# Performance work log

Hardware: AMD Instinct MI355X
Metric: run time of the kernel (lower is better)

The kernel has to match this reference:

```python
import jax, jax.numpy as jnp
import numpy as np

N = 100000
E = 1600000
C = 128
EPS = 1e-5


def setup_inputs() -> dict:
    key = jax.random.key(0)
    ks = jax.random.split(key, 12)
    x = jax.random.normal(ks[0], (N, C), dtype=jnp.float32)
    edges = jax.random.randint(ks[1], (2, E), 0, N, dtype=jnp.int64)
    s = 1.0 / np.sqrt(C)
    return {
        "x": x,
        "edges": edges,
        # GCNConv params
        "W1": jax.random.uniform(ks[2], (C, C), jnp.float32, -s, s),
        "b1": jnp.zeros((C,), jnp.float32),
        # GraphNorm params (shared between the two calls, as in the module)
        "gn_w": jnp.ones((C,), jnp.float32),
        "gn_b": jnp.zeros((C,), jnp.float32),
        "gn_ms": jnp.ones((C,), jnp.float32),  # mean_scale alpha
        # GATConv params (heads=1)
        "Wg": jax.random.uniform(ks[3], (C, C), jnp.float32, -s, s),
        "bg": jnp.zeros((C,), jnp.float32),
        "att_src": jax.random.uniform(ks[4], (C,), jnp.float32, -s, s),
        "att_dst": jax.random.uniform(ks[5], (C,), jnp.float32, -s, s),
    }


def _leaky(x, slope):
    return jnp.where(x >= 0, x, slope * x)


def _gcn_conv(x, src, dst, W, b):
    # PyG GCNConv with self-loops already appended to (src, dst)
    h = x @ W  # [N, C]
    deg = jnp.zeros((N,), x.dtype).at[dst].add(1.0)
    dinv = jax.lax.rsqrt(deg)  # deg >= 1 thanks to self-loops
    norm = dinv[src] * dinv[dst]  # [E+N]
    out = jax.ops.segment_sum(h[src] * norm[:, None], dst, num_segments=N)
    return out + b


def _graph_norm(x, w, b, ms):
    # PyG GraphNorm, single graph: center by alpha*mean, scale by std
    mean = jnp.mean(x, axis=0)
    out = x - ms * mean
    var = jnp.mean(out * out, axis=0)
    return w * out * jax.lax.rsqrt(var + EPS) + b


def _gat_conv(x, src, dst, W, b, att_src, att_dst):
    # PyG GATConv, heads=1, self-loops already appended
    h = x @ W  # [N, C]
    a_s = jnp.sum(h * att_src, axis=-1)  # [N]
    a_d = jnp.sum(h * att_dst, axis=-1)  # [N]
    e = _leaky(a_s[src] + a_d[dst], 0.2)  # [E+N]
    m = jax.ops.segment_max(e, dst, num_segments=N)
    e = jnp.exp(e - m[dst])
    denom = jax.ops.segment_sum(e, dst, num_segments=N)
    alpha = e / denom[dst]
    out = jax.ops.segment_sum(h[src] * alpha[:, None], dst, num_segments=N)
    return out + b


def reference(x, edges, W1, b1, gn_w, gn_b, gn_ms, Wg, bg, att_src, att_dst):
    loops = jnp.arange(N, dtype=edges.dtype)
    src = jnp.concatenate([edges[0], loops])
    dst = jnp.concatenate([edges[1], loops])

    t = _gcn_conv(x, src, dst, W1, b1)
    t = _graph_norm(t, gn_w, gn_b, gn_ms)
    t = _leaky(t, 0.01)  # nn.LeakyReLU default slope
    x = x + t

    t = _gat_conv(x, src, dst, Wg, bg, att_src, att_dst)
    t = _graph_norm(t, gn_w, gn_b, gn_ms)
    t = _leaky(t, 0.01)
    x = x + t
    return x
```

## Files before the change

### kernel.cpp

```cpp
#include <hip/hip_runtime.h>
#include <math.h>

#define NN 100000
#define NE 1600000
#define CH 128
#define TOTE (NE + NN)
#define EPSV 1e-5f
#define NB 98
#define NGB 1563

typedef __attribute__((ext_vector_type(8))) short short8;
typedef __attribute__((ext_vector_type(4))) float floatx4;

__device__ __forceinline__ float lrelu(float v, float s) { return v < 0.f ? v * s : v; }

__device__ __forceinline__ unsigned short f2bf(float f) {
    unsigned int u = __float_as_uint(f);
    u += 0x7FFF + ((u >> 16) & 1);
    return (unsigned short)(u >> 16);
}
__device__ __forceinline__ float bflo(unsigned int u) { return __uint_as_float(u << 16); }
__device__ __forceinline__ float bfhi(unsigned int u) { return __uint_as_float(u & 0xFFFF0000u); }

__global__ void k_init(int* __restrict__ deg, int* __restrict__ cursor, float* __restrict__ stats) {
    int i = blockIdx.x * 256 + threadIdx.x;
    if (i < NN) { deg[i] = 1; cursor[i] = 0; }
    if (i < 4096) stats[i] = 0.f;
}

__global__ void k_count(const int* __restrict__ edges, int* __restrict__ deg) {
    int i = blockIdx.x * 256 + threadIdx.x;
    if (i < NE) atomicAdd(&deg[edges[NE + i]], 1);
}

__global__ void k_scan1(const int* __restrict__ deg, int* __restrict__ bsum, float* __restrict__ dinv) {
    __shared__ int red[256];
    int t = threadIdx.x;
    int base = blockIdx.x * 1024 + t * 4;
    int s = 0;
#pragma unroll
    for (int j = 0; j < 4; j++) {
        int i = base + j;
        if (i < NN) { int d = deg[i]; s += d; dinv[i] = rsqrtf((float)d); }
    }
    red[t] = s; __syncthreads();
    for (int off = 128; off > 0; off >>= 1) { if (t < off) red[t] += red[t + off]; __syncthreads(); }
    if (t == 0) bsum[blockIdx.x] = red[0];
}

__global__ void k_scan2(const int* __restrict__ bsum, int* __restrict__ boff) {
    if (threadIdx.x == 0) {
        int acc = 0;
        for (int b = 0; b < NB; b++) { boff[b] = acc; acc += bsum[b]; }
    }
}

__global__ void k_scan3(const int* __restrict__ deg, const int* __restrict__ boff, int* __restrict__ rowptr) {
    __shared__ int sc[256];
    int t = threadIdx.x;
    int base = blockIdx.x * 1024 + t * 4;
    int d[4];
#pragma unroll
    for (int j = 0; j < 4; j++) { int i = base + j; d[j] = (i < NN) ? deg[i] : 0; }
    int local = d[0] + d[1] + d[2] + d[3];
    sc[t] = local; __syncthreads();
    for (int off = 1; off < 256; off <<= 1) {
        int v = (t >= off) ? sc[t - off] : 0;
        __syncthreads();
        sc[t] += v;
        __syncthreads();
    }
    int run = sc[t] - local + boff[blockIdx.x];
#pragma unroll
    for (int j = 0; j < 4; j++) {
        int i = base + j;
        if (i < NN) { rowptr[i] = run; run += d[j]; }
    }
    if (blockIdx.x == 0 && t == 0) rowptr[NN] = TOTE;
}

__global__ void k_fill(const int* __restrict__ edges, const int* __restrict__ rowptr,
                       int* __restrict__ cursor, int* __restrict__ csr) {
    int i = blockIdx.x * 256 + threadIdx.x;
    if (i < NE) {
        int s = edges[i], d = edges[NE + i];
        int pos = atomicAdd(&cursor[d], 1);
        csr[rowptr[d] + pos] = s;
    } else if (i < TOTE) {
        int v = i - NE;
        int pos = atomicAdd(&cursor[v], 1);
        csr[rowptr[v] + pos] = v;
    }
}

__global__ void k_wswz(const float* __restrict__ W1, const float* __restrict__ Wg,
                       unsigned short* __restrict__ Wsw1, unsigned short* __restrict__ Wsw2) {
    int t = blockIdx.x * 256 + threadIdx.x;
    if (t >= 16384) return;
    int j = t & 7, lane = (t >> 3) & 63, ks = (t >> 9) & 3, nt = t >> 11;
    int k = ks * 32 + (lane >> 4) * 8 + j;
    int n = nt * 16 + (lane & 15);
    Wsw1[t] = f2bf(W1[k * CH + n]);
    Wsw2[t] = f2bf(Wg[k * CH + n]);
}

__launch_bounds__(256, 4)
__global__ void k_gemm1(const float* __restrict__ X, const unsigned short* __restrict__ Wsw,
                        unsigned short* __restrict__ H) {
    __shared__ __align__(16) short Xl[64 * 136];
    int t = threadIdx.x, wave = t >> 6, lane = t & 63;
    int row0 = blockIdx.x * 64;
    {
        int r = t >> 2, q = t & 3;
        int gr = row0 + r;
        const float* Xr = X + (size_t)gr * CH;
#pragma unroll
        for (int j = 0; j < 4; j++) {
            int c0 = q * 32 + j * 8;
            float4 v0 = {0.f,0.f,0.f,0.f}, v1 = {0.f,0.f,0.f,0.f};
            if (gr < NN) { v0 = *(const float4*)&Xr[c0]; v1 = *(const float4*)&Xr[c0 + 4]; }
            short8 s;
            s[0]=f2bf(v0.x); s[1]=f2bf(v0.y); s[2]=f2bf(v0.z); s[3]=f2bf(v0.w);
            s[4]=f2bf(v1.x); s[5]=f2bf(v1.y); s[6]=f2bf(v1.z); s[7]=f2bf(v1.w);
            *(short8*)&Xl[r * 136 + c0] = s;
        }
    }
    __syncthreads();
    floatx4 acc[8];
#pragma unroll
    for (int nt = 0; nt < 8; nt++) acc[nt] = (floatx4){0.f, 0.f, 0.f, 0.f};
    int arow = wave * 16 + (lane & 15);
    int koff = (lane >> 4) * 8;
#pragma unroll
    for (int ks = 0; ks < 4; ks++) {
        short8 af = *(short8*)&Xl[arow * 136 + ks * 32 + koff];
#pragma unroll
        for (int nt = 0; nt < 8; nt++) {
            short8 bf = *(const short8*)&Wsw[((nt * 4 + ks) * 64 + lane) * 8];
            acc[nt] = __builtin_amdgcn_mfma_f32_16x16x32_bf16(af, bf, acc[nt], 0, 0, 0);
        }
    }
    int orow0 = row0 + wave * 16 + (lane >> 4) * 4;
    int ocol = lane & 15;
#pragma unroll
    for (int nt = 0; nt < 8; nt++) {
#pragma unroll
        for (int r = 0; r < 4; r++) {
            int row = orow0 + r;
            if (row < NN) H[(size_t)row * CH + nt * 16 + ocol] = f2bf(acc[nt][r]);
        }
    }
}

__launch_bounds__(256)
__global__ void k_gcn_agg(const unsigned short* __restrict__ H, const int* __restrict__ csr,
                          const int* __restrict__ rowptr, const float* __restrict__ dinv,
                          const float* __restrict__ b1, unsigned short* __restrict__ T,
                          float* __restrict__ stats) {
    __shared__ float red_s[4][128], red_q[4][128];
    int t = threadIdx.x, wave = t >> 6, lane = t & 63;
    int g = lane >> 4, sl = lane & 15;
    float4 bb0 = *(const float4*)&b1[sl * 8];
    float4 bb1 = *(const float4*)&b1[sl * 8 + 4];
    float bias[8] = {bb0.x, bb0.y, bb0.z, bb0.w, bb1.x, bb1.y, bb1.z, bb1.w};
    float ssum[8], ssq[8];
#pragma unroll
    for (int j = 0; j < 8; j++) { ssum[j] = 0.f; ssq[j] = 0.f; }
    for (int node = blockIdx.x * 4 + wave; node < NN; node += gridDim.x * 4) {
        int beg = rowptr[node], end = rowptr[node + 1];
        float di = dinv[node];
        float acc[8];
#pragma unroll
        for (int j = 0; j < 8; j++) acc[j] = 0.f;
        int kk0 = beg + g;
        int s_cur = csr[kk0 < end ? kk0 : end - 1];
        for (int k = beg; k < end; k += 4) {
            int kn = k + 4 + g;
            int s_next = csr[kn < end ? kn : end - 1];
            bool valid = (k + g) < end;
            float w = valid ? dinv[s_cur] : 0.f;
            uint4 u = *(const uint4*)&H[(size_t)s_cur * CH + sl * 8];
            acc[0] = fmaf(w, bflo(u.x), acc[0]); acc[1] = fmaf(w, bfhi(u.x), acc[1]);
            acc[2] = fmaf(w, bflo(u.y), acc[2]); acc[3] = fmaf(w, bfhi(u.y), acc[3]);
            acc[4] = fmaf(w, bflo(u.z), acc[4]); acc[5] = fmaf(w, bfhi(u.z), acc[5]);
            acc[6] = fmaf(w, bflo(u.w), acc[6]); acc[7] = fmaf(w, bfhi(u.w), acc[7]);
            s_cur = s_next;
        }
#pragma unroll
        for (int j = 0; j < 8; j++) {
            acc[j] += __shfl_xor(acc[j], 16);
            acc[j] += __shfl_xor(acc[j], 32);
        }
        if (lane < 16) {
            short8 sv;
#pragma unroll
            for (int j = 0; j < 8; j++) {
                float tv = fmaf(di, acc[j], bias[j]);
                sv[j] = (short)f2bf(tv);
                ssum[j] += tv; ssq[j] = fmaf(tv, tv, ssq[j]);
            }
            *(short8*)&T[(size_t)node * CH + sl * 8] = sv;
        }
    }
    if (lane < 16) {
#pragma unroll
        for (int j = 0; j < 8; j++) { red_s[wave][sl * 8 + j] = ssum[j]; red_q[wave][sl * 8 + j] = ssq[j]; }
    }
    __syncthreads();
    if (t < 128) {
        float s = 0.f, q = 0.f;
        for (int w2 = 0; w2 < 4; w2++) { s += red_s[w2][t]; q += red_q[w2][t]; }
        float* bank = stats + (blockIdx.x & 7) * 256;
        atomicAdd(&bank[t], s);
        atomicAdd(&bank[128 + t], q);
    }
}

__global__ void k_fin(const float* __restrict__ stats, const float* __restrict__ gw,
                      const float* __restrict__ gb, const float* __restrict__ gms,
                      float* __restrict__ alpha, float* __restrict__ beta) {
    int c = threadIdx.x;
    float s = 0.f, q = 0.f;
    for (int b = 0; b < 8; b++) { s += stats[b * 256 + c]; q += stats[b * 256 + 128 + c]; }
    float mean = s * (1.f / NN);
    float ctr = gms[c] * mean;
    float var = q * (1.f / NN) - 2.f * ctr * mean + ctr * ctr;
    float al = gw[c] * rsqrtf(var + EPSV);
    alpha[c] = al;
    beta[c] = gb[c] - al * ctr;
}

__launch_bounds__(256, 4)
__global__ void k_gemm2(const float* __restrict__ X, const unsigned short* __restrict__ T,
                        const unsigned short* __restrict__ Wsw, const float* __restrict__ alpha,
                        const float* __restrict__ beta, const float* __restrict__ attS,
                        const float* __restrict__ attD, float* __restrict__ X1out,
                        unsigned short* __restrict__ H, float* __restrict__ a_s, float* __restrict__ a_d) {
    __shared__ __align__(16) short Xl[64 * 136];
    int t = threadIdx.x, wave = t >> 6, lane = t & 63;
    int row0 = blockIdx.x * 64;
    {
        int r = t >> 2, q = t & 3;
        int gr = row0 + r;
        size_t base = (size_t)gr * CH;
#pragma unroll
        for (int j = 0; j < 4; j++) {
            int c0 = q * 32 + j * 8;
            float4 v0 = {0.f,0.f,0.f,0.f}, v1 = {0.f,0.f,0.f,0.f};
            if (gr < NN) {
                float4 xv0 = *(const float4*)&X[base + c0];
                float4 xv1 = *(const float4*)&X[base + c0 + 4];
                uint4 tu = *(const uint4*)&T[base + c0];
                float4 al0 = *(const float4*)&alpha[c0];
                float4 al1 = *(const float4*)&alpha[c0 + 4];
                float4 be0 = *(const float4*)&beta[c0];
                float4 be1 = *(const float4*)&beta[c0 + 4];
                v0.x = xv0.x + lrelu(fmaf(al0.x, bflo(tu.x), be0.x), 0.01f);
                v0.y = xv0.y + lrelu(fmaf(al0.y, bfhi(tu.x), be0.y), 0.01f);
                v0.z = xv0.z + lrelu(fmaf(al0.z, bflo(tu.y), be0.z), 0.01f);
                v0.w = xv0.w + lrelu(fmaf(al0.w, bfhi(tu.y), be0.w), 0.01f);
                v1.x = xv1.x + lrelu(fmaf(al1.x, bflo(tu.z), be1.x), 0.01f);
                v1.y = xv1.y + lrelu(fmaf(al1.y, bfhi(tu.z), be1.y), 0.01f);
                v1.z = xv1.z + lrelu(fmaf(al1.z, bflo(tu.w), be1.z), 0.01f);
                v1.w = xv1.w + lrelu(fmaf(al1.w, bfhi(tu.w), be1.w), 0.01f);
                *(float4*)&X1out[base + c0] = v0;
                *(float4*)&X1out[base + c0 + 4] = v1;
            }
            short8 s;
            s[0]=f2bf(v0.x); s[1]=f2bf(v0.y); s[2]=f2bf(v0.z); s[3]=f2bf(v0.w);
            s[4]=f2bf(v1.x); s[5]=f2bf(v1.y); s[6]=f2bf(v1.z); s[7]=f2bf(v1.w);
            *(short8*)&Xl[r * 136 + c0] = s;
        }
    }
    __syncthreads();
    floatx4 acc[8];
#pragma unroll
    for (int nt = 0; nt < 8; nt++) acc[nt] = (floatx4){0.f, 0.f, 0.f, 0.f};
    int arow = wave * 16 + (lane & 15);
    int koff = (lane >> 4) * 8;
#pragma unroll
    for (int ks = 0; ks < 4; ks++) {
        short8 af = *(short8*)&Xl[arow * 136 + ks * 32 + koff];
#pragma unroll
        for (int nt = 0; nt < 8; nt++) {
            short8 bf = *(const short8*)&Wsw[((nt * 4 + ks) * 64 + lane) * 8];
            acc[nt] = __builtin_amdgcn_mfma_f32_16x16x32_bf16(af, bf, acc[nt], 0, 0, 0);
        }
    }
    int orow0 = row0 + wave * 16 + (lane >> 4) * 4;
    int ocol = lane & 15;
    float ps[4] = {0.f, 0.f, 0.f, 0.f}, pd[4] = {0.f, 0.f, 0.f, 0.f};
#pragma unroll
    for (int nt = 0; nt < 8; nt++) {
        float as_v = attS[nt * 16 + ocol];
        float ad_v = attD[nt * 16 + ocol];
#pragma unroll
        for (int r = 0; r < 4; r++) {
            int row = orow0 + r;
            if (row < NN) H[(size_t)row * CH + nt * 16 + ocol] = f2bf(acc[nt][r]);
            ps[r] = fmaf(acc[nt][r], as_v, ps[r]);
            pd[r] = fmaf(acc[nt][r], ad_v, pd[r]);
        }
    }
#pragma unroll
    for (int off = 1; off < 16; off <<= 1) {
#pragma unroll
        for (int r = 0; r < 4; r++) {
            ps[r] += __shfl_xor(ps[r], off);
            pd[r] += __shfl_xor(pd[r], off);
        }
    }
    if ((lane & 15) == 0) {
#pragma unroll
        for (int r = 0; r < 4; r++) {
            int row = orow0 + r;
            if (row < NN) { a_s[row] = ps[r]; a_d[row] = pd[r]; }
        }
    }
}

__launch_bounds__(256)
__global__ void k_gat_agg(const unsigned short* __restrict__ H, const int* __restrict__ csr,
                          const int* __restrict__ rowptr, const float* __restrict__ a_s,
                          const float* __restrict__ a_d, const float* __restrict__ bg,
                          unsigned short* __restrict__ T, float* __restrict__ stats) {
    __shared__ float red_s[4][128], red_q[4][128];
    int t = threadIdx.x, wave = t >> 6, lane = t & 63;
    int g = lane >> 4, sl = lane & 15;
    float4 bb0 = *(const float4*)&bg[sl * 8];
    float4 bb1 = *(const float4*)&bg[sl * 8 + 4];
    float bias[8] = {bb0.x, bb0.y, bb0.z, bb0.w, bb1.x, bb1.y, bb1.z, bb1.w};
    float ssum[8], ssq[8];
#pragma unroll
    for (int j = 0; j < 8; j++) { ssum[j] = 0.f; ssq[j] = 0.f; }
    for (int node = blockIdx.x * 4 + wave; node < NN; node += gridDim.x * 4) {
        int beg = rowptr[node], end = rowptr[node + 1];
        float adI = a_d[node];
        float acc[8];
#pragma unroll
        for (int j = 0; j < 8; j++) acc[j] = 0.f;
        float den = 0.f;
        int kk0 = beg + g;
        int s_cur = csr[kk0 < end ? kk0 : end - 1];
        for (int k = beg; k < end; k += 4) {
            int kn = k + 4 + g;
            int s_next = csr[kn < end ? kn : end - 1];
            bool valid = (k + g) < end;
            float e = lrelu(a_s[s_cur] + adI, 0.2f);
            float wgt = valid ? __expf(e) : 0.f;
            den += wgt;
            uint4 u = *(const uint4*)&H[(size_t)s_cur * CH + sl * 8];
            acc[0] = fmaf(wgt, bflo(u.x), acc[0]); acc[1] = fmaf(wgt, bfhi(u.x), acc[1]);
            acc[2] = fmaf(wgt, bflo(u.y), acc[2]); acc[3] = fmaf(wgt, bfhi(u.y), acc[3]);
            acc[4] = fmaf(wgt, bflo(u.z), acc[4]); acc[5] = fmaf(wgt, bfhi(u.z), acc[5]);
            acc[6] = fmaf(wgt, bflo(u.w), acc[6]); acc[7] = fmaf(wgt, bfhi(u.w), acc[7]);
            s_cur = s_next;
        }
#pragma unroll
        for (int j = 0; j < 8; j++) {
            acc[j] += __shfl_xor(acc[j], 16);
            acc[j] += __shfl_xor(acc[j], 32);
        }
        den += __shfl_xor(den, 16);
        den += __shfl_xor(den, 32);
        float inv = 1.f / den;
        if (lane < 16) {
            short8 sv;
#pragma unroll
            for (int j = 0; j < 8; j++) {
                float tv = fmaf(acc[j], inv, bias[j]);
                sv[j] = (short)f2bf(tv);
                ssum[j] += tv; ssq[j] = fmaf(tv, tv, ssq[j]);
            }
            *(short8*)&T[(size_t)node * CH + sl * 8] = sv;
        }
    }
    if (lane < 16) {
#pragma unroll
        for (int j = 0; j < 8; j++) { red_s[wave][sl * 8 + j] = ssum[j]; red_q[wave][sl * 8 + j] = ssq[j]; }
    }
    __syncthreads();
    if (t < 128) {
        float s = 0.f, q = 0.f;
        for (int w2 = 0; w2 < 4; w2++) { s += red_s[w2][t]; q += red_q[w2][t]; }
        float* bank = stats + (blockIdx.x & 7) * 256;
        atomicAdd(&bank[t], s);
        atomicAdd(&bank[128 + t], q);
    }
}

__global__ void k_final(const unsigned short* __restrict__ T, const float* __restrict__ alpha,
                        const float* __restrict__ beta, float* __restrict__ out) {
    size_t i = (size_t)(blockIdx.x * 256 + threadIdx.x) * 4;
    if (i >= (size_t)NN * CH) return;
    int c = (int)(i & (CH - 1));
    uint2 tu = *(const uint2*)&T[i];
    float4 av = *(const float4*)&alpha[c];
    float4 bv = *(const float4*)&beta[c];
    float4 o = *(float4*)&out[i];
    o.x += lrelu(fmaf(av.x, bflo(tu.x), bv.x), 0.01f);
    o.y += lrelu(fmaf(av.y, bfhi(tu.x), bv.y), 0.01f);
    o.z += lrelu(fmaf(av.z, bflo(tu.y), bv.z), 0.01f);
    o.w += lrelu(fmaf(av.w, bfhi(tu.y), bv.w), 0.01f);
    *(float4*)&out[i] = o;
}

extern "C" void kernel_launch(void* const* d_in, const int* in_sizes, int n_in,
                              void* d_out, int out_size, void* d_ws, size_t ws_size,
                              hipStream_t stream) {
    const float* x    = (const float*)d_in[0];
    const int*   edges= (const int*)d_in[1];
    const float* W1   = (const float*)d_in[2];
    const float* b1   = (const float*)d_in[3];
    const float* gw   = (const float*)d_in[4];
    const float* gb   = (const float*)d_in[5];
    const float* gms  = (const float*)d_in[6];
    const float* Wg   = (const float*)d_in[7];
    const float* bg   = (const float*)d_in[8];
    const float* attS = (const float*)d_in[9];
    const float* attD = (const float*)d_in[10];
    float* out = (float*)d_out;

    char* w = (char*)d_ws;
    size_t o = 0;
    unsigned short* H = (unsigned short*)(w + o); o += (size_t)NN * CH * 2;
    unsigned short* T = (unsigned short*)(w + o); o += (size_t)NN * CH * 2;
    int*   csr    = (int*)(w + o);   o += (size_t)TOTE * 4;
    int*   rowptr = (int*)(w + o);   o += (size_t)(NN + 64) * 4;
    int*   deg    = (int*)(w + o);   o += (size_t)NN * 4;
    int*   cursor = (int*)(w + o);   o += (size_t)NN * 4;
    float* dinv   = (float*)(w + o); o += (size_t)NN * 4;
    float* a_s    = (float*)(w + o); o += (size_t)NN * 4;
    float* a_d    = (float*)(w + o); o += (size_t)NN * 4;
    int*   bsum   = (int*)(w + o);   o += 512;
    int*   boff   = (int*)(w + o);   o += 512;
    float* stats  = (float*)(w + o); o += 4096 * 4;
    float* alpha1 = (float*)(w + o); o += 512;
    float* beta1  = (float*)(w + o); o += 512;
    float* alpha2 = (float*)(w + o); o += 512;
    float* beta2  = (float*)(w + o); o += 512;
    unsigned short* Wsw1 = (unsigned short*)(w + o); o += 16384 * 2;
    unsigned short* Wsw2 = (unsigned short*)(w + o); o += 16384 * 2;

    k_init <<<(NN + 255) / 256, 256, 0, stream>>>(deg, cursor, stats);
    k_count<<<(NE + 255) / 256, 256, 0, stream>>>(edges, deg);
    k_scan1<<<NB, 256, 0, stream>>>(deg, bsum, dinv);
    k_scan2<<<1, 32, 0, stream>>>(bsum, boff);
    k_scan3<<<NB, 256, 0, stream>>>(deg, boff, rowptr);
    k_fill <<<(TOTE + 255) / 256, 256, 0, stream>>>(edges, rowptr, cursor, csr);
    k_wswz <<<64, 256, 0, stream>>>(W1, Wg, Wsw1, Wsw2);

    k_gemm1  <<<NGB, 256, 0, stream>>>(x, Wsw1, H);
    k_gcn_agg<<<2048, 256, 0, stream>>>(H, csr, rowptr, dinv, b1, T, stats);
    k_fin    <<<1, 128, 0, stream>>>(stats, gw, gb, gms, alpha1, beta1);

    k_gemm2  <<<NGB, 256, 0, stream>>>(x, T, Wsw2, alpha1, beta1, attS, attD, out, H, a_s, a_d);
    k_gat_agg<<<2048, 256, 0, stream>>>(H, csr, rowptr, a_s, a_d, bg, T, stats + 2048);
    k_fin    <<<1, 128, 0, stream>>>(stats + 2048, gw, gb, gms, alpha2, beta2);

    k_final<<<(NN * CH / 4 + 255) / 256, 256, 0, stream>>>(T, alpha2, beta2, out);
}
```

Before: 525.2 us.

## Widen aggregation gathers, vectorize CSR build, cache bf16 x for second GEMM

```diff
diff --git a/kernel.cpp b/kernel.cpp
--- a/kernel.cpp
+++ b/kernel.cpp
@@ -11,6 +11,7 @@
 
 typedef __attribute__((ext_vector_type(8))) short short8;
 typedef __attribute__((ext_vector_type(4))) float floatx4;
+typedef __attribute__((ext_vector_type(4))) int intx4;
 
 __device__ __forceinline__ float lrelu(float v, float s) { return v < 0.f ? v * s : v; }
 
@@ -30,7 +31,12 @@
 
 __global__ void k_count(const int* __restrict__ edges, int* __restrict__ deg) {
     int i = blockIdx.x * 256 + threadIdx.x;
-    if (i < NE) atomicAdd(&deg[edges[NE + i]], 1);
+    int base = i * 4;
+    if (base < NE) {
+        intx4 d = __builtin_nontemporal_load((const intx4*)&edges[NE + base]);
+        atomicAdd(&deg[d.x], 1); atomicAdd(&deg[d.y], 1);
+        atomicAdd(&deg[d.z], 1); atomicAdd(&deg[d.w], 1);
+    }
 }
 
 __global__ void k_scan1(const int* __restrict__ deg, int* __restrict__ bsum, float* __restrict__ dinv) {
@@ -49,10 +55,17 @@
 }
 
 __global__ void k_scan2(const int* __restrict__ bsum, int* __restrict__ boff) {
-    if (threadIdx.x == 0) {
-        int acc = 0;
-        for (int b = 0; b < NB; b++) { boff[b] = acc; acc += bsum[b]; }
-    }
+    __shared__ int sc[128];
+    int t = threadIdx.x;
+    int v = (t < NB) ? bsum[t] : 0;
+    sc[t] = v; __syncthreads();
+    for (int off = 1; off < 128; off <<= 1) {
+        int u = (t >= off) ? sc[t - off] : 0;
+        __syncthreads();
+        sc[t] += u;
+        __syncthreads();
+    }
+    if (t < NB) boff[t] = sc[t] - v;
 }
 
 __global__ void k_scan3(const int* __restrict__ deg, const int* __restrict__ boff, int* __restrict__ rowptr) {
@@ -80,16 +93,27 @@
 }
 
 __global__ void k_fill(const int* __restrict__ edges, const int* __restrict__ rowptr,
-                       int* __restrict__ cursor, int* __restrict__ csr) {
+                       int* __restrict__ cursor, int* __restrict__ csr, int lo, int hi) {
     int i = blockIdx.x * 256 + threadIdx.x;
-    if (i < NE) {
-        int s = edges[i], d = edges[NE + i];
-        int pos = atomicAdd(&cursor[d], 1);
-        csr[rowptr[d] + pos] = s;
-    } else if (i < TOTE) {
-        int v = i - NE;
-        int pos = atomicAdd(&cursor[v], 1);
-        csr[rowptr[v] + pos] = v;
+    int base = i * 4;
+    if (base < NE) {
+        intx4 d = __builtin_nontemporal_load((const intx4*)&edges[NE + base]);
+        intx4 s = __builtin_nontemporal_load((const intx4*)&edges[base]);
+#pragma unroll
+        for (int j = 0; j < 4; j++) {
+            int dj = (j == 0) ? d.x : (j == 1) ? d.y : (j == 2) ? d.z : d.w;
+            int sj = (j == 0) ? s.x : (j == 1) ? s.y : (j == 2) ? s.z : s.w;
+            if (dj >= lo && dj < hi) {
+                int pos = atomicAdd(&cursor[dj], 1);
+                csr[rowptr[dj] + pos] = sj;
+            }
+        }
+    } else {
+        int v = i - NE / 4;
+        if (v < NN && v >= lo && v < hi) {
+            int pos = atomicAdd(&cursor[v], 1);
+            csr[rowptr[v] + pos] = v;
+        }
     }
 }
 
@@ -106,7 +130,7 @@
 
 __launch_bounds__(256, 4)
 __global__ void k_gemm1(const float* __restrict__ X, const unsigned short* __restrict__ Wsw,
-                        unsigned short* __restrict__ H) {
+                        unsigned short* __restrict__ H, unsigned short* __restrict__ Xb) {
     __shared__ __align__(16) short Xl[64 * 136];
     int t = threadIdx.x, wave = t >> 6, lane = t & 63;
     int row0 = blockIdx.x * 64;
@@ -123,6 +147,7 @@
             s[0]=f2bf(v0.x); s[1]=f2bf(v0.y); s[2]=f2bf(v0.z); s[3]=f2bf(v0.w);
             s[4]=f2bf(v1.x); s[5]=f2bf(v1.y); s[6]=f2bf(v1.z); s[7]=f2bf(v1.w);
             *(short8*)&Xl[r * 136 + c0] = s;
+            if (gr < NN) *(short8*)&Xb[(size_t)gr * CH + c0] = s;
         }
     }
     __syncthreads();
@@ -159,52 +184,74 @@
                           float* __restrict__ stats) {
     __shared__ float red_s[4][128], red_q[4][128];
     int t = threadIdx.x, wave = t >> 6, lane = t & 63;
-    int g = lane >> 4, sl = lane & 15;
-    float4 bb0 = *(const float4*)&b1[sl * 8];
-    float4 bb1 = *(const float4*)&b1[sl * 8 + 4];
-    float bias[8] = {bb0.x, bb0.y, bb0.z, bb0.w, bb1.x, bb1.y, bb1.z, bb1.w};
-    float ssum[8], ssq[8];
-#pragma unroll
-    for (int j = 0; j < 8; j++) { ssum[j] = 0.f; ssq[j] = 0.f; }
+    int g = lane >> 3, sl = lane & 7;
+    float bias[16];
+    {
+        float4 b0 = *(const float4*)&b1[sl * 16];
+        float4 b1v = *(const float4*)&b1[sl * 16 + 4];
+        float4 b2 = *(const float4*)&b1[sl * 16 + 8];
+        float4 b3 = *(const float4*)&b1[sl * 16 + 12];
+        bias[0]=b0.x; bias[1]=b0.y; bias[2]=b0.z; bias[3]=b0.w;
+        bias[4]=b1v.x; bias[5]=b1v.y; bias[6]=b1v.z; bias[7]=b1v.w;
+        bias[8]=b2.x; bias[9]=b2.y; bias[10]=b2.z; bias[11]=b2.w;
+        bias[12]=b3.x; bias[13]=b3.y; bias[14]=b3.z; bias[15]=b3.w;
+    }
+    float ssum[16], ssq[16];
+#pragma unroll
+    for (int j = 0; j < 16; j++) { ssum[j] = 0.f; ssq[j] = 0.f; }
     for (int node = blockIdx.x * 4 + wave; node < NN; node += gridDim.x * 4) {
         int beg = rowptr[node], end = rowptr[node + 1];
         float di = dinv[node];
-        float acc[8];
-#pragma unroll
-        for (int j = 0; j < 8; j++) acc[j] = 0.f;
+        float acc[16];
+#pragma unroll
+        for (int j = 0; j < 16; j++) acc[j] = 0.f;
         int kk0 = beg + g;
         int s_cur = csr[kk0 < end ? kk0 : end - 1];
-        for (int k = beg; k < end; k += 4) {
-            int kn = k + 4 + g;
+        for (int k = beg; k < end; k += 8) {
+            int kn = k + 8 + g;
             int s_next = csr[kn < end ? kn : end - 1];
             bool valid = (k + g) < end;
             float w = valid ? dinv[s_cur] : 0.f;
-            uint4 u = *(const uint4*)&H[(size_t)s_cur * CH + sl * 8];
-            acc[0] = fmaf(w, bflo(u.x), acc[0]); acc[1] = fmaf(w, bfhi(u.x), acc[1]);
-            acc[2] = fmaf(w, bflo(u.y), acc[2]); acc[3] = fmaf(w, bfhi(u.y), acc[3]);
-            acc[4] = fmaf(w, bflo(u.z), acc[4]); acc[5] = fmaf(w, bfhi(u.z), acc[5]);
-            acc[6] = fmaf(w, bflo(u.w), acc[6]); acc[7] = fmaf(w, bfhi(u.w), acc[7]);
+            const unsigned short* Hp = &H[(size_t)s_cur * CH + sl * 16];
+            uint4 u0 = *(const uint4*)Hp;
+            uint4 u1 = *(const uint4*)(Hp + 8);
+            acc[0] = fmaf(w, bflo(u0.x), acc[0]);  acc[1] = fmaf(w, bfhi(u0.x), acc[1]);
+            acc[2] = fmaf(w, bflo(u0.y), acc[2]);  acc[3] = fmaf(w, bfhi(u0.y), acc[3]);
+            acc[4] = fmaf(w, bflo(u0.z), acc[4]);  acc[5] = fmaf(w, bfhi(u0.z), acc[5]);
+            acc[6] = fmaf(w, bflo(u0.w), acc[6]);  acc[7] = fmaf(w, bfhi(u0.w), acc[7]);
+            acc[8] = fmaf(w, bflo(u1.x), acc[8]);  acc[9] = fmaf(w, bfhi(u1.x), acc[9]);
+            acc[10] = fmaf(w, bflo(u1.y), acc[10]); acc[11] = fmaf(w, bfhi(u1.y), acc[11]);
+            acc[12] = fmaf(w, bflo(u1.z), acc[12]); acc[13] = fmaf(w, bfhi(u1.z), acc[13]);
+            acc[14] = fmaf(w, bflo(u1.w), acc[14]); acc[15] = fmaf(w, bfhi(u1.w), acc[15]);
             s_cur = s_next;
         }
 #pragma unroll
-        for (int j = 0; j < 8; j++) {
+        for (int j = 0; j < 16; j++) {
+            acc[j] += __shfl_xor(acc[j], 8);
             acc[j] += __shfl_xor(acc[j], 16);
             acc[j] += __shfl_xor(acc[j], 32);
         }
-        if (lane < 16) {
-            short8 sv;
+        if (g == 0) {
+            short8 sv0, sv1;
 #pragma unroll
             for (int j = 0; j < 8; j++) {
                 float tv = fmaf(di, acc[j], bias[j]);
-                sv[j] = (short)f2bf(tv);
+                sv0[j] = (short)f2bf(tv);
                 ssum[j] += tv; ssq[j] = fmaf(tv, tv, ssq[j]);
             }
-            *(short8*)&T[(size_t)node * CH + sl * 8] = sv;
-        }
-    }
-    if (lane < 16) {
-#pragma unroll
-        for (int j = 0; j < 8; j++) { red_s[wave][sl * 8 + j] = ssum[j]; red_q[wave][sl * 8 + j] = ssq[j]; }
+#pragma unroll
+            for (int j = 0; j < 8; j++) {
+                float tv = fmaf(di, acc[8 + j], bias[8 + j]);
+                sv1[j] = (short)f2bf(tv);
+                ssum[8 + j] += tv; ssq[8 + j] = fmaf(tv, tv, ssq[8 + j]);
+            }
+            *(short8*)&T[(size_t)node * CH + sl * 16] = sv0;
+            *(short8*)&T[(size_t)node * CH + sl * 16 + 8] = sv1;
+        }
+    }
+    if (g == 0) {
+#pragma unroll
+        for (int j = 0; j < 16; j++) { red_s[wave][sl * 16 + j] = ssum[j]; red_q[wave][sl * 16 + j] = ssq[j]; }
     }
     __syncthreads();
     if (t < 128) {
@@ -231,7 +278,7 @@
 }
 
 __launch_bounds__(256, 4)
-__global__ void k_gemm2(const float* __restrict__ X, const unsigned short* __restrict__ T,
+__global__ void k_gemm2(const unsigned short* __restrict__ Xb, const unsigned short* __restrict__ T,
                         const unsigned short* __restrict__ Wsw, const float* __restrict__ alpha,
                         const float* __restrict__ beta, const float* __restrict__ attS,
                         const float* __restrict__ attD, float* __restrict__ X1out,
@@ -246,29 +293,32 @@
 #pragma unroll
         for (int j = 0; j < 4; j++) {
             int c0 = q * 32 + j * 8;
-            float4 v0 = {0.f,0.f,0.f,0.f}, v1 = {0.f,0.f,0.f,0.f};
+            float v[8];
+#pragma unroll
+            for (int m = 0; m < 8; m++) v[m] = 0.f;
             if (gr < NN) {
-                float4 xv0 = *(const float4*)&X[base + c0];
-                float4 xv1 = *(const float4*)&X[base + c0 + 4];
+                uint4 xu = *(const uint4*)&Xb[base + c0];
                 uint4 tu = *(const uint4*)&T[base + c0];
                 float4 al0 = *(const float4*)&alpha[c0];
                 float4 al1 = *(const float4*)&alpha[c0 + 4];
                 float4 be0 = *(const float4*)&beta[c0];
                 float4 be1 = *(const float4*)&beta[c0 + 4];
-                v0.x = xv0.x + lrelu(fmaf(al0.x, bflo(tu.x), be0.x), 0.01f);
-                v0.y = xv0.y + lrelu(fmaf(al0.y, bfhi(tu.x), be0.y), 0.01f);
-                v0.z = xv0.z + lrelu(fmaf(al0.z, bflo(tu.y), be0.z), 0.01f);
-                v0.w = xv0.w + lrelu(fmaf(al0.w, bfhi(tu.y), be0.w), 0.01f);
-                v1.x = xv1.x + lrelu(fmaf(al1.x, bflo(tu.z), be1.x), 0.01f);
-                v1.y = xv1.y + lrelu(fmaf(al1.y, bfhi(tu.z), be1.y), 0.01f);
-                v1.z = xv1.z + lrelu(fmaf(al1.z, bflo(tu.w), be1.z), 0.01f);
-                v1.w = xv1.w + lrelu(fmaf(al1.w, bfhi(tu.w), be1.w), 0.01f);
-                *(float4*)&X1out[base + c0] = v0;
-                *(float4*)&X1out[base + c0 + 4] = v1;
+                v[0] = bflo(xu.x) + lrelu(fmaf(al0.x, bflo(tu.x), be0.x), 0.01f);
+                v[1] = bfhi(xu.x) + lrelu(fmaf(al0.y, bfhi(tu.x), be0.y), 0.01f);
+                v[2] = bflo(xu.y) + lrelu(fmaf(al0.z, bflo(tu.y), be0.z), 0.01f);
+                v[3] = bfhi(xu.y) + lrelu(fmaf(al0.w, bfhi(tu.y), be0.w), 0.01f);
+                v[4] = bflo(xu.z) + lrelu(fmaf(al1.x, bflo(tu.z), be1.x), 0.01f);
+                v[5] = bfhi(xu.z) + lrelu(fmaf(al1.y, bfhi(tu.z), be1.y), 0.01f);
+                v[6] = bflo(xu.w) + lrelu(fmaf(al1.z, bflo(tu.w), be1.z), 0.01f);
+                v[7] = bfhi(xu.w) + lrelu(fmaf(al1.w, bfhi(tu.w), be1.w), 0.01f);
+                float4 o0 = {v[0], v[1], v[2], v[3]};
+                float4 o1 = {v[4], v[5], v[6], v[7]};
+                *(float4*)&X1out[base + c0] = o0;
+                *(float4*)&X1out[base + c0 + 4] = o1;
             }
             short8 s;
-            s[0]=f2bf(v0.x); s[1]=f2bf(v0.y); s[2]=f2bf(v0.z); s[3]=f2bf(v0.w);
-            s[4]=f2bf(v1.x); s[5]=f2bf(v1.y); s[6]=f2bf(v1.z); s[7]=f2bf(v1.w);
+#pragma unroll
+            for (int m = 0; m < 8; m++) s[m] = (short)f2bf(v[m]);
             *(short8*)&Xl[r * 136 + c0] = s;
         }
     }
@@ -326,58 +376,81 @@
                           unsigned short* __restrict__ T, float* __restrict__ stats) {
     __shared__ float red_s[4][128], red_q[4][128];
     int t = threadIdx.x, wave = t >> 6, lane = t & 63;
-    int g = lane >> 4, sl = lane & 15;
-    float4 bb0 = *(const float4*)&bg[sl * 8];
-    float4 bb1 = *(const float4*)&bg[sl * 8 + 4];
-    float bias[8] = {bb0.x, bb0.y, bb0.z, bb0.w, bb1.x, bb1.y, bb1.z, bb1.w};
-    float ssum[8], ssq[8];
-#pragma unroll
-    for (int j = 0; j < 8; j++) { ssum[j] = 0.f; ssq[j] = 0.f; }
+    int g = lane >> 3, sl = lane & 7;
+    float bias[16];
+    {
+        float4 b0 = *(const float4*)&bg[sl * 16];
+        float4 b1v = *(const float4*)&bg[sl * 16 + 4];
+        float4 b2 = *(const float4*)&bg[sl * 16 + 8];
+        float4 b3 = *(const float4*)&bg[sl * 16 + 12];
+        bias[0]=b0.x; bias[1]=b0.y; bias[2]=b0.z; bias[3]=b0.w;
+        bias[4]=b1v.x; bias[5]=b1v.y; bias[6]=b1v.z; bias[7]=b1v.w;
+        bias[8]=b2.x; bias[9]=b2.y; bias[10]=b2.z; bias[11]=b2.w;
+        bias[12]=b3.x; bias[13]=b3.y; bias[14]=b3.z; bias[15]=b3.w;
+    }
+    float ssum[16], ssq[16];
+#pragma unroll
+    for (int j = 0; j < 16; j++) { ssum[j] = 0.f; ssq[j] = 0.f; }
     for (int node = blockIdx.x * 4 + wave; node < NN; node += gridDim.x * 4) {
         int beg = rowptr[node], end = rowptr[node + 1];
         float adI = a_d[node];
-        float acc[8];
-#pragma unroll
-        for (int j = 0; j < 8; j++) acc[j] = 0.f;
+        float acc[16];
+#pragma unroll
+        for (int j = 0; j < 16; j++) acc[j] = 0.f;
         float den = 0.f;
         int kk0 = beg + g;
         int s_cur = csr[kk0 < end ? kk0 : end - 1];
-        for (int k = beg; k < end; k += 4) {
-            int kn = k + 4 + g;
+        for (int k = beg; k < end; k += 8) {
+            int kn = k + 8 + g;
             int s_next = csr[kn < end ? kn : end - 1];
             bool valid = (k + g) < end;
             float e = lrelu(a_s[s_cur] + adI, 0.2f);
             float wgt = valid ? __expf(e) : 0.f;
             den += wgt;
-            uint4 u = *(const uint4*)&H[(size_t)s_cur * CH + sl * 8];
-            acc[0] = fmaf(wgt, bflo(u.x), acc[0]); acc[1] = fmaf(wgt, bfhi(u.x), acc[1]);
-            acc[2] = fmaf(wgt, bflo(u.y), acc[2]); acc[3] = fmaf(wgt, bfhi(u.y), acc[3]);
-            acc[4] = fmaf(wgt, bflo(u.z), acc[4]); acc[5] = fmaf(wgt, bfhi(u.z), acc[5]);
-            acc[6] = fmaf(wgt, bflo(u.w), acc[6]); acc[7] = fmaf(wgt, bfhi(u.w), acc[7]);
+            const unsigned short* Hp = &H[(size_t)s_cur * CH + sl * 16];
+            uint4 u0 = *(const uint4*)Hp;
+            uint4 u1 = *(const uint4*)(Hp + 8);
+            acc[0] = fmaf(wgt, bflo(u0.x), acc[0]);  acc[1] = fmaf(wgt, bfhi(u0.x), acc[1]);
+            acc[2] = fmaf(wgt, bflo(u0.y), acc[2]);  acc[3] = fmaf(wgt, bfhi(u0.y), acc[3]);
+            acc[4] = fmaf(wgt, bflo(u0.z), acc[4]);  acc[5] = fmaf(wgt, bfhi(u0.z), acc[5]);
+            acc[6] = fmaf(wgt, bflo(u0.w), acc[6]);  acc[7] = fmaf(wgt, bfhi(u0.w), acc[7]);
+            acc[8] = fmaf(wgt, bflo(u1.x), acc[8]);  acc[9] = fmaf(wgt, bfhi(u1.x), acc[9]);
+            acc[10] = fmaf(wgt, bflo(u1.y), acc[10]); acc[11] = fmaf(wgt, bfhi(u1.y), acc[11]);
+            acc[12] = fmaf(wgt, bflo(u1.z), acc[12]); acc[13] = fmaf(wgt, bfhi(u1.z), acc[13]);
+            acc[14] = fmaf(wgt, bflo(u1.w), acc[14]); acc[15] = fmaf(wgt, bfhi(u1.w), acc[15]);
             s_cur = s_next;
         }
 #pragma unroll
-        for (int j = 0; j < 8; j++) {
+        for (int j = 0; j < 16; j++) {
+            acc[j] += __shfl_xor(acc[j], 8);
             acc[j] += __shfl_xor(acc[j], 16);
             acc[j] += __shfl_xor(acc[j], 32);
         }
+        den += __shfl_xor(den, 8);
         den += __shfl_xor(den, 16);
         den += __shfl_xor(den, 32);
         float inv = 1.f / den;
-        if (lane < 16) {
-            short8 sv;
+        if (g == 0) {
+            short8 sv0, sv1;
 #pragma unroll
             for (int j = 0; j < 8; j++) {
                 float tv = fmaf(acc[j], inv, bias[j]);
-                sv[j] = (short)f2bf(tv);
+                sv0[j] = (short)f2bf(tv);
                 ssum[j] += tv; ssq[j] = fmaf(tv, tv, ssq[j]);
             }
-            *(short8*)&T[(size_t)node * CH + sl * 8] = sv;
-        }
-    }
-    if (lane < 16) {
-#pragma unroll
-        for (int j = 0; j < 8; j++) { red_s[wave][sl * 8 + j] = ssum[j]; red_q[wave][sl * 8 + j] = ssq[j]; }
+#pragma unroll
+            for (int j = 0; j < 8; j++) {
+                float tv = fmaf(acc[8 + j], inv, bias[8 + j]);
+                sv1[j] = (short)f2bf(tv);
+                ssum[8 + j] += tv; ssq[8 + j] = fmaf(tv, tv, ssq[8 + j]);
+            }
+            *(short8*)&T[(size_t)node * CH + sl * 16] = sv0;
+            *(short8*)&T[(size_t)node * CH + sl * 16 + 8] = sv1;
+        }
+    }
+    if (g == 0) {
+#pragma unroll
+        for (int j = 0; j < 16; j++) { red_s[wave][sl * 16 + j] = ssum[j]; red_q[wave][sl * 16 + j] = ssq[j]; }
     }
     __syncthreads();
     if (t < 128) {
@@ -423,8 +496,9 @@
 
     char* w = (char*)d_ws;
     size_t o = 0;
-    unsigned short* H = (unsigned short*)(w + o); o += (size_t)NN * CH * 2;
-    unsigned short* T = (unsigned short*)(w + o); o += (size_t)NN * CH * 2;
+    unsigned short* H  = (unsigned short*)(w + o); o += (size_t)NN * CH * 2;
+    unsigned short* T  = (unsigned short*)(w + o); o += (size_t)NN * CH * 2;
+    unsigned short* Xb = (unsigned short*)(w + o); o += (size_t)NN * CH * 2;
     int*   csr    = (int*)(w + o);   o += (size_t)TOTE * 4;
     int*   rowptr = (int*)(w + o);   o += (size_t)(NN + 64) * 4;
     int*   deg    = (int*)(w + o);   o += (size_t)NN * 4;
@@ -443,18 +517,20 @@
     unsigned short* Wsw2 = (unsigned short*)(w + o); o += 16384 * 2;
 
     k_init <<<(NN + 255) / 256, 256, 0, stream>>>(deg, cursor, stats);
-    k_count<<<(NE + 255) / 256, 256, 0, stream>>>(edges, deg);
+    k_count<<<(NE / 4 + 255) / 256, 256, 0, stream>>>(edges, deg);
     k_scan1<<<NB, 256, 0, stream>>>(deg, bsum, dinv);
-    k_scan2<<<1, 32, 0, stream>>>(bsum, boff);
+    k_scan2<<<1, 128, 0, stream>>>(bsum, boff);
     k_scan3<<<NB, 256, 0, stream>>>(deg, boff, rowptr);
-    k_fill <<<(TOTE + 255) / 256, 256, 0, stream>>>(edges, rowptr, cursor, csr);
+    int fillb = (NE / 4 + NN + 255) / 256;
+    k_fill <<<fillb, 256, 0, stream>>>(edges, rowptr, cursor, csr, 0, NN / 2);
+    k_fill <<<fillb, 256, 0, stream>>>(edges, rowptr, cursor, csr, NN / 2, NN);
     k_wswz <<<64, 256, 0, stream>>>(W1, Wg, Wsw1, Wsw2);
 
-    k_gemm1  <<<NGB, 256, 0, stream>>>(x, Wsw1, H);
+    k_gemm1  <<<NGB, 256, 0, stream>>>(x, Wsw1, H, Xb);
     k_gcn_agg<<<2048, 256, 0, stream>>>(H, csr, rowptr, dinv, b1, T, stats);
     k_fin    <<<1, 128, 0, stream>>>(stats, gw, gb, gms, alpha1, beta1);
 
-    k_gemm2  <<<NGB, 256, 0, stream>>>(x, T, Wsw2, alpha1, beta1, attS, attD, out, H, a_s, a_d);
+    k_gemm2  <<<NGB, 256, 0, stream>>>(Xb, T, Wsw2, alpha1, beta1, attS, attD, out, H, a_s, a_d);
     k_gat_agg<<<2048, 256, 0, stream>>>(H, csr, rowptr, a_s, a_d, bg, T, stats + 2048);
     k_fin    <<<1, 128, 0, stream>>>(stats + 2048, gw, gb, gms, alpha2, beta2);
 
```

Measured after the change: 554.4 us. 5.6% more time.
